# Performance work log

Measured on AMD Instinct MI355X. Metric: run time of the kernel, lower is better.

Reference implementation:

```python
import jax, jax.numpy as jnp
import numpy as np

# FCHL19 hyperparameters (from init_kwargs defaults)
NSPEC = 4
RCUT = 6.0
NRS2 = 24
NRS3 = 20
ETA2 = 0.32
ETA3 = 2.7
TWO_BODY_DECAY = 1.8
THREE_BODY_WEIGHT = float(np.sqrt(2.7 / np.pi) * 13.4)  # sqrt(eta3/pi)*13.4, as in __init__
THREE_BODY_DECAY = 0.57
PI = float(np.pi)
NPAIRS = NSPEC * (NSPEC + 1) // 2  # 10 unordered element pairs
RS2 = jnp.linspace(0.0, RCUT, NRS2 + 1)[1:]
RS3 = jnp.linspace(0.0, RCUT, NRS3 + 1)[1:]


def setup_inputs() -> dict:
    key = jax.random.key(0)
    k1, k2, k3 = jax.random.split(key, 3)
    B, A = 64, 48
    X = jax.random.uniform(k1, (B, A, 3), jnp.float32, 0.0, 12.0)  # coords in 12 A box
    Z = jax.random.randint(k2, (B, A), 0, NSPEC, dtype=jnp.int32)  # species indices into [1,6,7,8]
    atom_counts = jax.random.randint(k3, (B,), 24, A + 1, dtype=jnp.int32)
    atomIDs = (jnp.arange(B * A, dtype=jnp.int32) % A)
    molIDs = (jnp.arange(B * A, dtype=jnp.int32) // A)
    return {"X": X, "Z": Z, "atomIDs": atomIDs, "molIDs": molIDs, "atom_counts": atom_counts}


def _fchl_rep(X, Z, atom_counts):
    B, A, _ = X.shape
    idx = jnp.arange(A)
    valid = idx[None, :] < atom_counts[:, None]                       # [B,A]
    diff = X[:, :, None, :] - X[:, None, :, :]                        # [B,A,A,3] (X_i - X_j)
    r2 = jnp.sum(diff * diff, axis=-1)
    eye = jnp.eye(A, dtype=bool)
    pmask = valid[:, :, None] & valid[:, None, :] & ~eye              # [B,A,A]
    r = jnp.sqrt(jnp.where(pmask, r2, 1.0))
    within = pmask & (r < RCUT)
    rs = jnp.where(within, r, 1.0)                                    # safe distances
    fc = jnp.where(within, 0.5 * (jnp.cos(PI * rs / RCUT) + 1.0), 0.0)

    # ---- two-body: log-normal radial basis with power-law scaling ----
    s2 = jnp.log1p(ETA2 / (rs * rs))                                  # sigma^2
    mu = jnp.log(rs) - 0.5 * s2
    pref = fc / (rs ** TWO_BODY_DECAY) / (jnp.sqrt(s2) * np.sqrt(2.0 * PI))
    radial2 = (pref[..., None] / RS2) * jnp.exp(
        -(jnp.log(RS2) - mu[..., None]) ** 2 / (2.0 * s2[..., None]))  # [B,A,A,nRs2]
    eoh = jax.nn.one_hot(Z, NSPEC, dtype=X.dtype) * valid[..., None]  # [B,A,S]
    rep2 = jnp.einsum('bijk,bjs->bisk', radial2, eoh).reshape(B, A, NSPEC * NRS2)

    # ---- three-body: ATM-weighted radial x (cos,sin) angular, pairs k>j ----
    rij = rs[:, :, :, None]   # [B,A(i),A(j),1]
    rik = rs[:, :, None, :]   # [B,A(i),1,A(k)]
    rjk = rs[:, None, :, :]   # [B,1,A(j),A(k)]
    cos_i = jnp.einsum('bijx,bikx->bijk', diff, diff) / (rij * rik)
    cos_i = jnp.clip(cos_i, -1.0, 1.0)
    cos_j = (rij * rij + rjk * rjk - rik * rik) / (2.0 * rij * rjk)
    cos_k = (rik * rik + rjk * rjk - rij * rij) / (2.0 * rik * rjk)
    mask3 = (within[:, :, :, None] & within[:, :, None, :]
             & (idx[None, :] > idx[:, None])[None, None, :, :])        # k > j
    ksi3 = THREE_BODY_WEIGHT * (1.0 + 3.0 * cos_i * cos_j * cos_k) \
        / (rij * rik * rjk) ** THREE_BODY_DECAY
    w = jnp.where(mask3, ksi3 * fc[:, :, :, None] * fc[:, :, None, :], 0.0)
    wc = w * cos_i
    ws = w * jnp.sqrt(jnp.clip(1.0 - cos_i * cos_i, 0.0, 1.0))
    d = 0.5 * (rij + rik)                                             # [B,A,A,A]

    # unordered element-pair bin for (Z_j, Z_k)
    ej = Z[:, :, None]
    ek = Z[:, None, :]
    pmin = jnp.minimum(ej, ek)
    pmax = jnp.maximum(ej, ek)
    pidx = pmin * (2 * NSPEC - pmin - 1) // 2 + pmax                  # [B,A,A]
    poh = jax.nn.one_hot(pidx, NPAIRS, dtype=X.dtype)                 # [B,A,A,P]

    def step(carry, Rl):
        rad = jnp.exp(-ETA3 * (d - Rl) ** 2)
        rc = jnp.einsum('bijk,bjkp->bip', wc * rad, poh)
        rsn = jnp.einsum('bijk,bjkp->bip', ws * rad, poh)
        return carry, jnp.stack([rc, rsn], axis=-1)                   # [B,A,P,2]

    _, rep3 = jax.lax.scan(step, 0, RS3)                              # [nRs3,B,A,P,2]
    rep3 = jnp.transpose(rep3, (1, 2, 3, 0, 4)).reshape(B, A, NPAIRS * NRS3 * 2)
    return jnp.concatenate([rep2, rep3], axis=-1)                     # [B,A,496]


def reference(X, Z, atomIDs, molIDs, atom_counts):
    # atomIDs/molIDs are CUDA work-distribution lists; math-irrelevant here.
    return _fchl_rep(X, Z, atom_counts)
```

## Files before the change

kernel.cpp:

```cpp
#include <hip/hip_runtime.h>
#include <math.h>

#define B_MOL 64
#define A_MAX 48
#define NSPEC 4
#define NRS2 24
#define NRS3 20
#define NPAIRS 10
#define REP2 (NSPEC * NRS2)
#define REP3 (NPAIRS * NRS3 * 2)
#define REPTOT (REP2 + REP3)
#define TRIP_CAP 1084

#define RCUT_F 6.0f
#define ETA2_F 0.32f
#define ETA3_F 2.7f
#define PI_F 3.14159265358979323846f
#define W3_F 12.4225780586f
#define SQRT_2PI_F 2.5066282746310002f

__device__ __forceinline__ void decode_tri(int t, int m, int& a_out, int& c_out) {
    const float fm = (float)(2 * m - 1);
    const float disc = fm * fm - 8.0f * (float)t;
    const float sq = __builtin_amdgcn_sqrtf(disc);
    int a = (int)((fm - sq) * 0.5f);
    if (a < 0) a = 0;
    while (a > 0 && (a * (2 * m - 1 - a)) / 2 > t) --a;
    while (((a + 1) * (2 * m - 1 - (a + 1))) / 2 <= t) ++a;
    a_out = a;
    c_out = t - (a * (2 * m - 1 - a)) / 2 + a + 1;
}

__global__ __launch_bounds__(256) void fchl_kernel(
    const float* __restrict__ X, const int* __restrict__ Z,
    const int* __restrict__ atom_counts, float* __restrict__ out)
{
    const int bi = blockIdx.x;
    const int b = bi / A_MAX;
    const int i = bi % A_MAX;
    const int tid = threadIdx.x;

    __shared__ float sx[A_MAX], sy[A_MAX], sz[A_MAX];
    __shared__ int   sZa[A_MAX];
    __shared__ float nb_dx[A_MAX], nb_dy[A_MAX], nb_dz[A_MAX];
    __shared__ float nb_r[A_MAX], nb_r2[A_MAX], nb_rinv[A_MAX];
    __shared__ float nb_fc[A_MAX], nb_mu[A_MAX], nb_i2s2[A_MAX], nb_pref[A_MAX];
    __shared__ int   nb_z[A_MAX];
    __shared__ int   nb_m;
    __shared__ int   bcnt[NPAIRS], bstart[NPAIRS];
    __shared__ unsigned short pq[TRIP_CAP];
    __shared__ float4 trip[TRIP_CAP];

    const int cnt = atom_counts[b];

    if (tid < A_MAX) {
        sx[tid]  = X[(b * A_MAX + tid) * 3 + 0];
        sy[tid]  = X[(b * A_MAX + tid) * 3 + 1];
        sz[tid]  = X[(b * A_MAX + tid) * 3 + 2];
        sZa[tid] = Z[b * A_MAX + tid];
    }
    if (tid < NPAIRS) bcnt[tid] = 0;
    __syncthreads();

    const float xi = sx[i], yi = sy[i], zi = sz[i];
    const bool ivalid = (i < cnt);

    if (tid < 64) {
        const int j = tid;
        bool flag = false;
        float dx = 0.f, dy = 0.f, dz = 0.f, r = 1.f;
        if (j < A_MAX) {
            dx = xi - sx[j]; dy = yi - sy[j]; dz = zi - sz[j];
            r = __builtin_amdgcn_sqrtf(dx * dx + dy * dy + dz * dz);
            flag = ivalid && (j < cnt) && (j != i) && (r < RCUT_F);
        }
        const unsigned long long mask = __ballot(flag ? 1 : 0);
        if (flag) {
            const int pos = __popcll(mask & ((1ull << tid) - 1ull));
            nb_dx[pos] = dx; nb_dy[pos] = dy; nb_dz[pos] = dz;
            nb_r[pos]  = r;  nb_r2[pos] = r * r;
            nb_rinv[pos] = __builtin_amdgcn_rcpf(r);
            nb_z[pos]  = sZa[j];
            const float fc = 0.5f * (__cosf(PI_F * r * (1.0f / RCUT_F)) + 1.0f);
            const float lr = __logf(r);
            const float s2 = log1pf(ETA2_F / (r * r));
            nb_fc[pos]   = fc;
            nb_mu[pos]   = lr - 0.5f * s2;
            nb_i2s2[pos] = 0.5f * __builtin_amdgcn_rcpf(s2);
            nb_pref[pos] = fc * __expf(-1.8f * lr) *
                           __builtin_amdgcn_rcpf(__builtin_amdgcn_sqrtf(s2) * SQRT_2PI_F);
        }
        if (tid == 0) nb_m = (int)__popcll(mask);
    }
    __syncthreads();
    const int m = nb_m;
    const int ntrip = m * (m - 1) / 2;

    float* orow = out + (size_t)bi * REPTOT;

    for (int t = tid; t < ntrip; t += 256) {
        int a, c;
        decode_tri(t, m, a, c);
        const int zj = nb_z[a], zk = nb_z[c];
        const int pmn = min(zj, zk), pmx = max(zj, zk);
        const int p = (pmn * (2 * NSPEC - pmn - 1)) / 2 + pmx;
        const int q = atomicAdd(&bcnt[p], 1);
        pq[t] = (unsigned short)(p | (q << 4));
    }
    __syncthreads();
    if (tid == 0) {
        int s = 0;
        for (int p = 0; p < NPAIRS; ++p) { bstart[p] = s; s += bcnt[p]; }
    }
    __syncthreads();

    for (int t = tid; t < ntrip; t += 256) {
        int a, c;
        decode_tri(t, m, a, c);

        const float rij = nb_r[a], rik = nb_r[c];
        const float r2ij = nb_r2[a], r2ik = nb_r2[c];
        const float rinv_a = nb_rinv[a], rinv_c = nb_rinv[c];
        const float djx = nb_dx[a], djy = nb_dy[a], djz = nb_dz[a];
        const float dkx = nb_dx[c], dky = nb_dy[c], dkz = nb_dz[c];

        float cosi = (djx * dkx + djy * dky + djz * dkz) * rinv_a * rinv_c;
        cosi = fminf(1.0f, fmaxf(-1.0f, cosi));

        const float ex = dkx - djx, ey = dky - djy, ez = dkz - djz;
        const float rjk2 = ex * ex + ey * ey + ez * ez;
        const float rjk = __builtin_amdgcn_sqrtf(rjk2);
        const bool w_jk = (rjk < RCUT_F);
        const float rjke  = w_jk ? rjk : 1.0f;
        const float rjke2 = w_jk ? rjk2 : 1.0f;
        const float rinv_jk = w_jk ? __builtin_amdgcn_rcpf(rjk) : 1.0f;

        const float cosj = (r2ij + rjke2 - r2ik) * 0.5f * rinv_a * rinv_jk;
        const float cosk = (r2ik + rjke2 - r2ij) * 0.5f * rinv_c * rinv_jk;

        const float ksi = W3_F * (1.0f + 3.0f * cosi * cosj * cosk)
                        * __expf(-0.57f * __logf(rij * rik * rjke));
        const float w  = ksi * nb_fc[a] * nb_fc[c];
        const float wc = w * cosi;
        const float s1 = fmaxf(1.0f - cosi * cosi, 0.0f);
        const float ws = w * __builtin_amdgcn_sqrtf(s1);
        const float d  = 0.5f * (rij + rik);

        const unsigned short e = pq[t];
        const int slot = bstart[e & 15] + (int)(e >> 4);
        trip[slot] = make_float4(wc, ws, d, 0.0f);
    }
    __syncthreads();

    if (tid < NPAIRS * NRS3) {
        const int p = tid / NRS3;
        const int l = tid % NRS3;
        const float Rl = 0.3f * (float)(l + 1);
        const int s0 = bstart[p];
        const int s1 = s0 + bcnt[p];
        float ac = 0.0f, as_ = 0.0f;
        for (int s = s0; s < s1; ++s) {
            const float4 v = trip[s];
            const float dd = v.z - Rl;
            const float rad = __expf(-ETA3_F * dd * dd);
            ac  += v.x * rad;
            as_ += v.y * rad;
        }
        orow[REP2 + p * (NRS3 * 2) + l * 2 + 0] = ac;
        orow[REP2 + p * (NRS3 * 2) + l * 2 + 1] = as_;
    } else {
        for (int t2 = tid - 200; t2 < REP2; t2 += 56) {
            const int s = t2 / NRS2;
            const int n = t2 % NRS2;
            const float Rn = 0.25f * (float)(n + 1);
            const float logRn = __logf(Rn);
            float acc = 0.0f;
            for (int a = 0; a < m; ++a) {
                if (nb_z[a] == s) {
                    const float dmu = logRn - nb_mu[a];
                    acc += nb_pref[a] * __expf(-dmu * dmu * nb_i2s2[a]);
                }
            }
            orow[t2] = acc * __builtin_amdgcn_rcpf(Rn);
        }
    }
}

extern "C" void kernel_launch(void* const* d_in, const int* in_sizes, int n_in,
                              void* d_out, int out_size, void* d_ws, size_t ws_size,
                              hipStream_t stream) {
    const float* X           = (const float*)d_in[0];
    const int*   Z           = (const int*)d_in[1];
    const int*   atom_counts = (const int*)d_in[4];
    float* out = (float*)d_out;

    fchl_kernel<<<B_MOL * A_MAX, 256, 0, stream>>>(X, Z, atom_counts, out);
}
```

Baseline: 76.04 us.

## Early-exit invalid atoms, drop staging smem, split triplet SoA, pipeline reduction loads

```diff
diff --git a/kernel.cpp b/kernel.cpp
--- a/kernel.cpp
+++ b/kernel.cpp
@@ -31,7 +31,7 @@
     c_out = t - (a * (2 * m - 1 - a)) / 2 + a + 1;
 }
 
-__global__ __launch_bounds__(256) void fchl_kernel(
+__global__ __launch_bounds__(256, 8) void fchl_kernel(
     const float* __restrict__ X, const int* __restrict__ Z,
     const int* __restrict__ atom_counts, float* __restrict__ out)
 {
@@ -40,8 +40,6 @@
     const int i = bi % A_MAX;
     const int tid = threadIdx.x;
 
-    __shared__ float sx[A_MAX], sy[A_MAX], sz[A_MAX];
-    __shared__ int   sZa[A_MAX];
     __shared__ float nb_dx[A_MAX], nb_dy[A_MAX], nb_dz[A_MAX];
     __shared__ float nb_r[A_MAX], nb_r2[A_MAX], nb_rinv[A_MAX];
     __shared__ float nb_fc[A_MAX], nb_mu[A_MAX], nb_i2s2[A_MAX], nb_pref[A_MAX];
@@ -49,30 +47,34 @@
     __shared__ int   nb_m;
     __shared__ int   bcnt[NPAIRS], bstart[NPAIRS];
     __shared__ unsigned short pq[TRIP_CAP];
-    __shared__ float4 trip[TRIP_CAP];
+    __shared__ float trip_wc[TRIP_CAP], trip_ws[TRIP_CAP], trip_d[TRIP_CAP];
 
     const int cnt = atom_counts[b];
-
-    if (tid < A_MAX) {
-        sx[tid]  = X[(b * A_MAX + tid) * 3 + 0];
-        sy[tid]  = X[(b * A_MAX + tid) * 3 + 1];
-        sz[tid]  = X[(b * A_MAX + tid) * 3 + 2];
-        sZa[tid] = Z[b * A_MAX + tid];
-    }
+    float* orow = out + (size_t)bi * REPTOT;
+
+    if (i >= cnt) {
+        for (int t = tid; t < REPTOT; t += 256) orow[t] = 0.0f;
+        return;
+    }
+
     if (tid < NPAIRS) bcnt[tid] = 0;
-    __syncthreads();
-
-    const float xi = sx[i], yi = sy[i], zi = sz[i];
-    const bool ivalid = (i < cnt);
+
+    const float xi = X[(b * A_MAX + i) * 3 + 0];
+    const float yi = X[(b * A_MAX + i) * 3 + 1];
+    const float zi = X[(b * A_MAX + i) * 3 + 2];
 
     if (tid < 64) {
         const int j = tid;
         bool flag = false;
         float dx = 0.f, dy = 0.f, dz = 0.f, r = 1.f;
-        if (j < A_MAX) {
-            dx = xi - sx[j]; dy = yi - sy[j]; dz = zi - sz[j];
+        int zj = 0;
+        if (j < A_MAX && j < cnt) {
+            dx = xi - X[(b * A_MAX + j) * 3 + 0];
+            dy = yi - X[(b * A_MAX + j) * 3 + 1];
+            dz = zi - X[(b * A_MAX + j) * 3 + 2];
+            zj = Z[b * A_MAX + j];
             r = __builtin_amdgcn_sqrtf(dx * dx + dy * dy + dz * dz);
-            flag = ivalid && (j < cnt) && (j != i) && (r < RCUT_F);
+            flag = (j != i) && (r < RCUT_F);
         }
         const unsigned long long mask = __ballot(flag ? 1 : 0);
         if (flag) {
@@ -80,7 +82,7 @@
             nb_dx[pos] = dx; nb_dy[pos] = dy; nb_dz[pos] = dz;
             nb_r[pos]  = r;  nb_r2[pos] = r * r;
             nb_rinv[pos] = __builtin_amdgcn_rcpf(r);
-            nb_z[pos]  = sZa[j];
+            nb_z[pos]  = zj;
             const float fc = 0.5f * (__cosf(PI_F * r * (1.0f / RCUT_F)) + 1.0f);
             const float lr = __logf(r);
             const float s2 = log1pf(ETA2_F / (r * r));
@@ -96,8 +98,6 @@
     const int m = nb_m;
     const int ntrip = m * (m - 1) / 2;
 
-    float* orow = out + (size_t)bi * REPTOT;
-
     for (int t = tid; t < ntrip; t += 256) {
         int a, c;
         decode_tri(t, m, a, c);
@@ -108,9 +108,10 @@
         pq[t] = (unsigned short)(p | (q << 4));
     }
     __syncthreads();
-    if (tid == 0) {
+    if (tid < NPAIRS) {
         int s = 0;
-        for (int p = 0; p < NPAIRS; ++p) { bstart[p] = s; s += bcnt[p]; }
+        for (int p = 0; p < tid; ++p) s += bcnt[p];
+        bstart[tid] = s;
     }
     __syncthreads();
 
@@ -148,7 +149,7 @@
 
         const unsigned short e = pq[t];
         const int slot = bstart[e & 15] + (int)(e >> 4);
-        trip[slot] = make_float4(wc, ws, d, 0.0f);
+        trip_wc[slot] = wc; trip_ws[slot] = ws; trip_d[slot] = d;
     }
     __syncthreads();
 
@@ -159,12 +160,22 @@
         const int s0 = bstart[p];
         const int s1 = s0 + bcnt[p];
         float ac = 0.0f, as_ = 0.0f;
-        for (int s = s0; s < s1; ++s) {
-            const float4 v = trip[s];
-            const float dd = v.z - Rl;
+        if (s1 > s0) {
+            float wcv = trip_wc[s0], wsv = trip_ws[s0], dv = trip_d[s0];
+            for (int s = s0 + 1; s < s1; ++s) {
+                const float wcn = trip_wc[s];
+                const float wsn = trip_ws[s];
+                const float dn  = trip_d[s];
+                const float dd = dv - Rl;
+                const float rad = __expf(-ETA3_F * dd * dd);
+                ac  += wcv * rad;
+                as_ += wsv * rad;
+                wcv = wcn; wsv = wsn; dv = dn;
+            }
+            const float dd = dv - Rl;
             const float rad = __expf(-ETA3_F * dd * dd);
-            ac  += v.x * rad;
-            as_ += v.y * rad;
+            ac  += wcv * rad;
+            as_ += wsv * rad;
         }
         orow[REP2 + p * (NRS3 * 2) + l * 2 + 0] = ac;
         orow[REP2 + p * (NRS3 * 2) + l * 2 + 1] = as_;
```

Result: faster. 74.09 us (-2.6%).
